# Kernel tuning notes

Measured on AMD Instinct MI355X. Metric: run time of the kernel, lower is better.

The kernel has to match this reference:

```python
import jax, jax.numpy as jnp
import numpy as np

B, S, HID = 2, 2048, 2048
NH, NOPE, ROPE = 16, 128, 64
HD = NOPE + ROPE          # 192
VHD = 128
KVR, QR = 512, 1536
FFN = 5632
THETA = 10000.0
EPS = 1e-6


def rmsnorm(x, w, eps=EPS):
    xf = x.astype(jnp.float32)
    rms = jnp.sqrt(jnp.mean(xf * xf, axis=-1, keepdims=True) + eps)
    return (xf / rms).astype(x.dtype) * w


def apply_rope(x, cos, sin):
    # x: (..., rope_dim); half-split rotation convention
    half = x.shape[-1] // 2
    x1, x2 = x[..., :half], x[..., half:]
    return jnp.concatenate([x1 * cos - x2 * sin, x2 * cos + x1 * sin], axis=-1)


def rope_tables(seq_len, dim, theta=THETA):
    inv_freq = 1.0 / (theta ** (jnp.arange(0, dim, 2, dtype=jnp.float32) / dim))
    t = jnp.arange(seq_len, dtype=jnp.float32)
    freqs = jnp.outer(t, inv_freq)           # (S, dim/2)
    return jnp.cos(freqs), jnp.sin(freqs)


def setup_inputs():
    key = jax.random.key(0)
    ks = jax.random.split(key, 10)
    def w(k, shape, fan_in):
        return jax.random.normal(k, shape, dtype=jnp.float32) * (fan_in ** -0.5)
    return {
        'x': jax.random.normal(ks[0], (B, S, HID), dtype=jnp.float32),
        'attn_norm_w': jnp.ones((HID,), jnp.float32),
        'wq_down': w(ks[1], (HID, QR), HID),
        'wq_up': w(ks[2], (QR, NH * HD), QR),
        'wkv_down': w(ks[3], (HID, KVR + ROPE), HID),
        'kv_norm_w': jnp.ones((KVR,), jnp.float32),
        'wkv_up': w(ks[4], (KVR, NH * (NOPE + VHD)), KVR),
        'wout': w(ks[5], (NH * VHD, HID), NH * VHD),
        'ffn_norm_w': jnp.ones((HID,), jnp.float32),
        'w_gate': w(ks[6], (HID, FFN), HID),
        'w_up': w(ks[7], (HID, FFN), HID),
        'w_down': w(ks[8], (FFN, HID), FFN),
    }


def reference(x, attn_norm_w, wq_down, wq_up, wkv_down, kv_norm_w, wkv_up, wout,
              ffn_norm_w, w_gate, w_up, w_down):
    scale = 1.0 / np.sqrt(HD)
    # --- attention sub-block ---
    h = rmsnorm(x, attn_norm_w)
    q = (h @ wq_down) @ wq_up                       # (B,S,NH*HD)
    q = q.reshape(B, S, NH, HD)
    q_nope, q_rope = q[..., :NOPE], q[..., NOPE:]
    kv_full = h @ wkv_down                          # (B,S,KVR+ROPE)
    kv_c, k_rope = kv_full[..., :KVR], kv_full[..., KVR:]
    kv_c = rmsnorm(kv_c, kv_norm_w)
    kv_exp = (kv_c @ wkv_up).reshape(B, S, NH, NOPE + VHD)
    k_nope, v = kv_exp[..., :NOPE], kv_exp[..., NOPE:]

    cos, sin = rope_tables(S, ROPE)                 # (S, ROPE/2)
    cos4, sin4 = cos[None, :, None, :], sin[None, :, None, :]
    q_rope = apply_rope(q_rope, cos4, sin4)         # (B,S,NH,ROPE)
    k_rope = apply_rope(k_rope[:, :, None, :], cos4, sin4)  # (B,S,1,ROPE)
    k_rope = jnp.broadcast_to(k_rope, (B, S, NH, ROPE))

    q_full = jnp.concatenate([q_nope, q_rope], axis=-1)     # (B,S,NH,HD)
    k = jnp.concatenate([k_nope, k_rope], axis=-1)          # (B,S,NH,HD)

    scores = jnp.einsum('bqhd,bkhd->bhqk', q_full, k) * scale
    causal = jnp.tril(jnp.ones((S, S), dtype=bool))
    scores = jnp.where(causal[None, None], scores, jnp.finfo(scores.dtype).min)
    probs = jax.nn.softmax(scores, axis=-1)
    attn = jnp.einsum('bhqk,bkhd->bqhd', probs, v).reshape(B, S, NH * VHD)
    x = x + attn @ wout

    # --- SwiGLU MLP sub-block ---
    h2 = rmsnorm(x, ffn_norm_w)
    ffn = (jax.nn.silu(h2 @ w_gate) * (h2 @ w_up)) @ w_down
    return x + ffn
```

## Files before the change

kernel.cpp:

```cpp
#include <hip/hip_runtime.h>
#include <hip/hip_bf16.h>


using bf16x8 = __attribute__((ext_vector_type(8))) short;
using f32x4  = __attribute__((ext_vector_type(4))) float;

#define GLOBAL_AS __attribute__((address_space(1)))
#define LDS_AS    __attribute__((address_space(3)))
#define MFMA16(a, b, c) __builtin_amdgcn_mfma_f32_16x16x32_bf16((a), (b), (c), 0, 0, 0)

static constexpr int Sc = 2048;

__device__ __forceinline__ void gload16(const void* g, void* l) {
  __builtin_amdgcn_global_load_lds((const GLOBAL_AS unsigned int*)g,
                                   (LDS_AS unsigned int*)l, 16, 0, 0);
}
__device__ __forceinline__ float bf2f(unsigned short u) {
  union { float f; unsigned int i; } x; x.i = ((unsigned int)u) << 16; return x.f;
}
__device__ __forceinline__ unsigned short f2bf(float f) {
  union { float f; unsigned int i; } x; x.f = f;
  unsigned int i = x.i;
  return (unsigned short)((i + 0x7fffu + ((i >> 16) & 1u)) >> 16);
}
__device__ __forceinline__ int swz4(int r) { return ((r >> 2) & 3) ^ (r & 3); }

__global__ void fill_k(float* out, float v, int n) {
  int i = blockIdx.x * 256 + threadIdx.x;
  if (i < n) out[i] = v;
}

__global__ __launch_bounds__(256) void wtrans(const float* __restrict__ W,
                                              unsigned short* __restrict__ WT,
                                              int K, int N) {
  __shared__ float t[64][65];
  const int n0 = blockIdx.x * 64, k0 = blockIdx.y * 64;
  const int tx = threadIdx.x & 15, ty = threadIdx.x >> 4;
#pragma unroll
  for (int i = 0; i < 4; ++i) {
    int k = k0 + ty + i * 16;
    const float4 v = *(const float4*)(W + (size_t)k * N + n0 + tx * 4);
    t[ty + i * 16][tx * 4 + 0] = v.x;
    t[ty + i * 16][tx * 4 + 1] = v.y;
    t[ty + i * 16][tx * 4 + 2] = v.z;
    t[ty + i * 16][tx * 4 + 3] = v.w;
  }
  __syncthreads();
  const int kx = threadIdx.x & 7, ny = threadIdx.x >> 3;
#pragma unroll
  for (int i = 0; i < 2; ++i) {
    int nl = ny + i * 32;
    unsigned short u[8];
#pragma unroll
    for (int j = 0; j < 8; ++j) u[j] = f2bf(t[kx * 8 + j][nl]);
    *(uint4*)(WT + (size_t)(n0 + nl) * K + k0 + kx * 8) = *(uint4*)u;
  }
}

__global__ void rope_tab(float* __restrict__ cosT, float* __restrict__ sinT) {
  int i = blockIdx.x * 256 + threadIdx.x;
  if (i >= Sc * 32) return;
  int s = i >> 5, j = i & 31;
  float inv = powf(10000.0f, -(float)j / 32.0f);
  float a = (float)s * inv;
  cosT[i] = cosf(a);
  sinT[i] = sinf(a);
}

__global__ __launch_bounds__(256) void rmsnorm_k(const float* __restrict__ in,
                                                 const float* __restrict__ w,
                                                 unsigned short* __restrict__ out,
                                                 int D, int istride, int ostride) {
  const int row = blockIdx.x;
  const float* x = in + (size_t)row * istride;
  float ss = 0.f;
  for (int c = threadIdx.x * 4; c < D; c += 1024) {
    const float4 v = *(const float4*)(x + c);
    ss += v.x * v.x + v.y * v.y + v.z * v.z + v.w * v.w;
  }
#pragma unroll
  for (int off = 1; off < 64; off <<= 1) ss += __shfl_xor(ss, off);
  __shared__ float part[4];
  if ((threadIdx.x & 63) == 0) part[threadIdx.x >> 6] = ss;
  __syncthreads();
  float tot = part[0] + part[1] + part[2] + part[3];
  float r = rsqrtf(tot / (float)D + 1e-6f);
  for (int c = threadIdx.x * 4; c < D; c += 1024) {
    const float4 v = *(const float4*)(x + c);
    ushort4 o;
    o.x = f2bf(v.x * r * w[c + 0]);
    o.y = f2bf(v.y * r * w[c + 1]);
    o.z = f2bf(v.z * r * w[c + 2]);
    o.w = f2bf(v.w * r * w[c + 3]);
    *(ushort4*)(out + (size_t)row * ostride + c) = o;
  }
}

enum { EPI_BF16 = 0, EPI_F32 = 1, EPI_ADDF32 = 2, EPI_SILU = 3 };

template <int EPI>
__global__ __launch_bounds__(256) void gemm_sb1(const unsigned short* __restrict__ A,
                                                const unsigned short* __restrict__ BT,
                                                void* __restrict__ Cp,
                                                const float* __restrict__ resid,
                                                const unsigned short* __restrict__ other,
                                                int M, int N, int K) {
  __shared__ unsigned short ldsA[128 * 64];
  __shared__ unsigned short ldsB[128 * 64];
  const int tid = threadIdx.x;
  const int w = tid >> 6, lane = tid & 63;
  const int rl = lane & 15, gh = lane >> 4;
  const int wm = (w >> 1) * 64, wn = (w & 1) * 64;

  const int nwg = gridDim.x;
  const int orig = blockIdx.x;
  const int qq = nwg >> 3, rr = nwg & 7;
  const int xcd = orig & 7, lidx = orig >> 3;
  const int fswz = (xcd < rr ? xcd * (qq + 1) : rr * (qq + 1) + (xcd - rr) * qq) + lidx;
  const int MT = M >> 7;
  const int m0 = (fswz % MT) * 128;
  const int n0 = (fswz / MT) * 128;

  const unsigned short* sA[4];
  const unsigned short* sB[4];
#pragma unroll
  for (int i = 0; i < 4; ++i) {
    int G = i * 256 + tid, r = G >> 3, sl = (G & 7) ^ (r & 7);
    sA[i] = A + (size_t)(m0 + r) * K + sl * 8;
    sB[i] = BT + (size_t)(n0 + r) * K + sl * 8;
  }
  auto STAGE = [&](int kt) {
    const int ko = kt * 64;
#pragma unroll
    for (int i = 0; i < 4; ++i) {
      gload16(sA[i] + ko, &ldsA[(i * 256 + w * 64) * 8]);
      gload16(sB[i] + ko, &ldsB[(i * 256 + w * 64) * 8]);
    }
  };

  int aoff[4], boff[4];
#pragma unroll
  for (int i = 0; i < 4; ++i) {
    aoff[i] = (wm + i * 16 + rl) * 64;
    boff[i] = (wn + i * 16 + rl) * 64;
  }

  f32x4 acc[4][4] = {};
  const int nk = K >> 6;

  STAGE(0);
  asm volatile("s_waitcnt vmcnt(0)" ::: "memory");
  __builtin_amdgcn_s_barrier();

  for (int kt = 0; kt < nk; ++kt) {
    bf16x8 a[4][2], b[4][2];
#pragma unroll
    for (int i = 0; i < 4; ++i)
#pragma unroll
      for (int ks = 0; ks < 2; ++ks) {
        const int ra = wm + i * 16 + rl;
        a[i][ks] = *(const bf16x8*)&ldsA[aoff[i] + ((((ks << 2) + gh)) ^ (ra & 7)) * 8];
        const int rb = wn + i * 16 + rl;
        b[i][ks] = *(const bf16x8*)&ldsB[boff[i] + ((((ks << 2) + gh)) ^ (rb & 7)) * 8];
      }
    asm volatile("s_waitcnt lgkmcnt(0)" ::: "memory");
    __builtin_amdgcn_sched_barrier(0);
    __builtin_amdgcn_s_setprio(1);
#pragma unroll
    for (int i = 0; i < 4; ++i)
#pragma unroll
      for (int j = 0; j < 4; ++j) acc[i][j] = MFMA16(a[i][0], b[j][0], acc[i][j]);
    __builtin_amdgcn_s_setprio(0);
    __builtin_amdgcn_sched_barrier(0);
    __builtin_amdgcn_s_barrier();
    STAGE((kt + 1 < nk) ? kt + 1 : nk - 1);
    __builtin_amdgcn_sched_barrier(0);
    __builtin_amdgcn_s_setprio(1);
#pragma unroll
    for (int i = 0; i < 4; ++i)
#pragma unroll
      for (int j = 0; j < 4; ++j) acc[i][j] = MFMA16(a[i][1], b[j][1], acc[i][j]);
    __builtin_amdgcn_s_setprio(0);
    __builtin_amdgcn_sched_barrier(0);
    asm volatile("s_waitcnt vmcnt(0)" ::: "memory");
    __builtin_amdgcn_s_barrier();
  }

#pragma unroll
  for (int i = 0; i < 4; ++i) {
#pragma unroll
    for (int j = 0; j < 4; ++j) {
#pragma unroll
      for (int rg = 0; rg < 4; ++rg) {
        const int row = m0 + wm + i * 16 + gh * 4 + rg;
        const int col = n0 + wn + j * 16 + rl;
        const size_t idx = (size_t)row * N + col;
        const float v = acc[i][j][rg];
        if constexpr (EPI == EPI_BF16) {
          ((unsigned short*)Cp)[idx] = f2bf(v);
        } else if constexpr (EPI == EPI_F32) {
          ((float*)Cp)[idx] = v;
        } else if constexpr (EPI == EPI_ADDF32) {
          ((float*)Cp)[idx] = v + resid[idx];
        } else {
          float gv = bf2f(other[idx]);
          float sg = gv / (1.f + __expf(-gv));
          ((unsigned short*)Cp)[idx] = f2bf(sg * v);
        }
      }
    }
  }
}

template <int EPI>
__global__ __launch_bounds__(512) void gemm_sb2(const unsigned short* __restrict__ A,
                                                const unsigned short* __restrict__ BT,
                                                void* __restrict__ Cp,
                                                const float* __restrict__ resid,
                                                const unsigned short* __restrict__ other,
                                                int M, int N, int K) {
  __shared__ unsigned short ldsA[128 * 64];
  __shared__ unsigned short ldsB[256 * 64];
  const int tid = threadIdx.x;
  const int w = tid >> 6, lane = tid & 63;
  const int rl = lane & 15, gh = lane >> 4;
  const int wm = (w >> 2) * 64, wn = (w & 3) * 64;

  const int nwg = gridDim.x;
  const int orig = blockIdx.x;
  const int qq = nwg >> 3, rr = nwg & 7;
  const int xcd = orig & 7, lidx = orig >> 3;
  const int fswz = (xcd < rr ? xcd * (qq + 1) : rr * (qq + 1) + (xcd - rr) * qq) + lidx;
  const int MT = M >> 7;
  const int m0 = (fswz % MT) * 128;
  const int n0 = (fswz / MT) * 256;

  const unsigned short* sA[2];
#pragma unroll
  for (int i = 0; i < 2; ++i) {
    int G = i * 512 + tid, r = G >> 3, sl = (G & 7) ^ (r & 7);
    sA[i] = A + (size_t)(m0 + r) * K + sl * 8;
  }
  const unsigned short* sB[4];
#pragma unroll
  for (int i = 0; i < 4; ++i) {
    int G = i * 512 + tid, r = G >> 3, sl = (G & 7) ^ (r & 7);
    sB[i] = BT + (size_t)(n0 + r) * K + sl * 8;
  }
  auto STAGE = [&](int kt) {
    const int ko = kt * 64;
#pragma unroll
    for (int i = 0; i < 2; ++i)
      gload16(sA[i] + ko, &ldsA[(i * 512 + w * 64) * 8]);
#pragma unroll
    for (int i = 0; i < 4; ++i)
      gload16(sB[i] + ko, &ldsB[(i * 512 + w * 64) * 8]);
  };

  int aoff[4], boff[4];
#pragma unroll
  for (int i = 0; i < 4; ++i) {
    aoff[i] = (wm + i * 16 + rl) * 64;
    boff[i] = (wn + i * 16 + rl) * 64;
  }

  f32x4 acc[4][4] = {};
  const int nk = K >> 6;

  STAGE(0);
  asm volatile("s_waitcnt vmcnt(0)" ::: "memory");
  __builtin_amdgcn_s_barrier();

  for (int kt = 0; kt < nk; ++kt) {
    bf16x8 a[4][2], b[4][2];
#pragma unroll
    for (int i = 0; i < 4; ++i)
#pragma unroll
      for (int ks = 0; ks < 2; ++ks) {
        const int ra = wm + i * 16 + rl;
        a[i][ks] = *(const bf16x8*)&ldsA[aoff[i] + ((((ks << 2) + gh)) ^ (ra & 7)) * 8];
        const int rb = wn + i * 16 + rl;
        b[i][ks] = *(const bf16x8*)&ldsB[boff[i] + ((((ks << 2) + gh)) ^ (rb & 7)) * 8];
      }
    asm volatile("s_waitcnt lgkmcnt(0)" ::: "memory");
    __builtin_amdgcn_sched_barrier(0);
    __builtin_amdgcn_s_setprio(1);
#pragma unroll
    for (int i = 0; i < 4; ++i)
#pragma unroll
      for (int j = 0; j < 4; ++j) acc[i][j] = MFMA16(a[i][0], b[j][0], acc[i][j]);
    __builtin_amdgcn_s_setprio(0);
    __builtin_amdgcn_sched_barrier(0);
    __builtin_amdgcn_s_barrier();
    STAGE((kt + 1 < nk) ? kt + 1 : nk - 1);
    __builtin_amdgcn_sched_barrier(0);
    __builtin_amdgcn_s_setprio(1);
#pragma unroll
    for (int i = 0; i < 4; ++i)
#pragma unroll
      for (int j = 0; j < 4; ++j) acc[i][j] = MFMA16(a[i][1], b[j][1], acc[i][j]);
    __builtin_amdgcn_s_setprio(0);
    __builtin_amdgcn_sched_barrier(0);
    asm volatile("s_waitcnt vmcnt(0)" ::: "memory");
    __builtin_amdgcn_s_barrier();
  }

#pragma unroll
  for (int i = 0; i < 4; ++i) {
#pragma unroll
    for (int j = 0; j < 4; ++j) {
#pragma unroll
      for (int rg = 0; rg < 4; ++rg) {
        const int row = m0 + wm + i * 16 + gh * 4 + rg;
        const int col = n0 + wn + j * 16 + rl;
        const size_t idx = (size_t)row * N + col;
        const float v = acc[i][j][rg];
        if constexpr (EPI == EPI_BF16) {
          ((unsigned short*)Cp)[idx] = f2bf(v);
        } else if constexpr (EPI == EPI_F32) {
          ((float*)Cp)[idx] = v;
        } else if constexpr (EPI == EPI_ADDF32) {
          ((float*)Cp)[idx] = v + resid[idx];
        } else {
          float gv = bf2f(other[idx]);
          float sg = gv / (1.f + __expf(-gv));
          ((unsigned short*)Cp)[idx] = f2bf(sg * v);
        }
      }
    }
  }
}

__global__ __launch_bounds__(256) void repack_q(const unsigned short* __restrict__ q,
                                                const float* __restrict__ cosT,
                                                const float* __restrict__ sinT,
                                                unsigned short* __restrict__ Qc) {
  const int row = blockIdx.x;
  const int b = row >> 11, s = row & 2047;
  const float scale = 0.07216878364870322f;
  const unsigned short* qr = q + (size_t)row * 3072;
  for (int i = threadIdx.x; i < 3072; i += 256) {
    int h = i / 192, d = i - h * 192;
    float v;
    if (d < 128) {
      v = bf2f(qr[h * 192 + d]);
    } else {
      int j = d - 128;
      int jj = j & 31;
      float x1 = bf2f(qr[h * 192 + 128 + jj]);
      float x2 = bf2f(qr[h * 192 + 160 + jj]);
      float c = cosT[s * 32 + jj], sn = sinT[s * 32 + jj];
      v = (j < 32) ? (x1 * c - x2 * sn) : (x2 * c + x1 * sn);
    }
    Qc[((size_t)(b * 16 + h) * Sc + s) * 192 + d] = f2bf(v * scale);
  }
}

__global__ __launch_bounds__(256) void repack_kv(const unsigned short* __restrict__ kvex,
                                                 const float* __restrict__ kvf,
                                                 const float* __restrict__ cosT,
                                                 const float* __restrict__ sinT,
                                                 unsigned short* __restrict__ Kc,
                                                 unsigned short* __restrict__ VT) {
  __shared__ unsigned short vt_lds[32][136];
  const int bid = blockIdx.x;
  const int st = bid & 63;
  const int h = (bid >> 6) & 15;
  const int b = bid >> 10;
  const int s0 = st * 32;
  const int tid = threadIdx.x;
  const size_t KcBase = (size_t)(b * 16 + h) * Sc;
  for (int i = tid; i < 32 * 32; i += 256) {
    int r = i >> 5, g = i & 31;
    uint4 vdat = *(const uint4*)(kvex + (size_t)(b * Sc + s0 + r) * 4096 + h * 256 + g * 8);
    if (g < 16) {
      *(uint4*)(Kc + (KcBase + s0 + r) * 192 + g * 8) = vdat;
    } else {
      *(uint4*)(&vt_lds[r][(g - 16) * 8]) = vdat;
    }
  }
  for (int i = tid; i < 32 * 64; i += 256) {
    int r = i >> 6, d = i & 63;
    int s = s0 + r;
    int jj = d & 31;
    const float* kvrow = kvf + (size_t)(b * Sc + s) * 640;
    float x1 = kvrow[512 + jj], x2 = kvrow[544 + jj];
    float c = cosT[s * 32 + jj], sn = sinT[s * 32 + jj];
    float v = (d < 32) ? (x1 * c - x2 * sn) : (x2 * c + x1 * sn);
    Kc[(KcBase + s) * 192 + 128 + d] = f2bf(v);
  }
  __syncthreads();
  const int f = tid >> 1, sh = (tid & 1) * 16;
  unsigned int vals[8];
#pragma unroll
  for (int k2 = 0; k2 < 8; ++k2) {
    unsigned int lo = vt_lds[sh + 2 * k2][f];
    unsigned int hi = vt_lds[sh + 2 * k2 + 1][f];
    vals[k2] = lo | (hi << 16);
  }
  unsigned short* dst = VT + ((size_t)(b * 16 + h) * 128 + f) * Sc + s0 + sh;
  ((uint4*)dst)[0] = make_uint4(vals[0], vals[1], vals[2], vals[3]);
  ((uint4*)dst)[1] = make_uint4(vals[4], vals[5], vals[6], vals[7]);
}

__global__ __launch_bounds__(512) void attn_k(const unsigned short* __restrict__ Qc,
                                              const unsigned short* __restrict__ Kc,
                                              const unsigned short* __restrict__ VT,
                                              unsigned short* __restrict__ Ob) {
  __shared__ unsigned short lds_k[2][64 * 192];
  __shared__ unsigned short lds_v[2][128 * 64];
  __shared__ __align__(16) unsigned short p_lds[8][16 * 72];
  const int tid = threadIdx.x, w = tid >> 6, lane = tid & 63;
  const int rl = lane & 15, gh = lane >> 4;
  const int bidx = blockIdx.x;
  const int bh = bidx & 31;
  const int qt = 15 - (bidx >> 5);
  const unsigned short* Qh = Qc + (size_t)bh * Sc * 192;
  const unsigned short* Kh = Kc + (size_t)bh * Sc * 192;
  const unsigned short* Vh = VT + (size_t)bh * 128 * Sc;
  const int qr0 = qt * 128 + w * 16;

  bf16x8 qf[6];
#pragma unroll
  for (int kk = 0; kk < 6; ++kk)
    qf[kk] = *(const bf16x8*)(Qh + (size_t)(qr0 + rl) * 192 + kk * 32 + gh * 8);

  f32x4 o[8] = {};
  float mrun[4] = {-1e30f, -1e30f, -1e30f, -1e30f};
  float srun[4] = {0.f, 0.f, 0.f, 0.f};

  int kr[3], kg[3];
#pragma unroll
  for (int j = 0; j < 3; ++j) {
    int G = j * 512 + tid;
    int r = G / 24, gq = G - r * 24;
    kr[j] = r;
    kg[j] = (gq & ~7) | ((gq & 7) ^ (r & 7));
  }
  int vr[2], vg[2];
#pragma unroll
  for (int j = 0; j < 2; ++j) {
    int G = j * 512 + tid;
    int r = G >> 3;
    vr[j] = r;
    vg[j] = (G & 7) ^ (r & 7);
  }

  auto STAGE = [&](int t, int b) {
    const int k0 = t * 64;
#pragma unroll
    for (int j = 0; j < 3; ++j)
      gload16(Kh + (size_t)(k0 + kr[j]) * 192 + kg[j] * 8,
              &lds_k[b][(j * 512 + w * 64) * 8]);
#pragma unroll
    for (int j = 0; j < 2; ++j)
      gload16(Vh + (size_t)vr[j] * Sc + k0 + vg[j] * 8,
              &lds_v[b][(j * 512 + w * 64) * 8]);
  };

  STAGE(0, 0);
  asm volatile("s_waitcnt vmcnt(0)" ::: "memory");
  __builtin_amdgcn_s_barrier();
  __builtin_amdgcn_sched_barrier(0);

  const int nt = 2 * qt + 2;
  int cur = 0;
  for (int t = 0; t < nt; ++t) {
    if (t + 1 < nt) STAGE(t + 1, cur ^ 1);
    const int k0 = t * 64;
    if (k0 <= qr0 + 15) {
      const unsigned short* lk = lds_k[cur];
      const unsigned short* lv = lds_v[cur];
      f32x4 s[4] = {};
      __builtin_amdgcn_s_setprio(1);
#pragma unroll
      for (int kk = 0; kk < 6; ++kk) {
        const int gq = kk * 4 + gh;
#pragma unroll
        for (int ks = 0; ks < 4; ++ks) {
          const int krow = ks * 16 + rl;
          const int ph = (gq & ~7) | ((gq & 7) ^ (krow & 7));
          bf16x8 kf = *(const bf16x8*)&lk[krow * 192 + ph * 8];
          s[ks] = MFMA16(qf[kk], kf, s[ks]);
        }
      }
      __builtin_amdgcn_s_setprio(0);
      if (k0 + 63 > qr0) {
#pragma unroll
        for (int ks = 0; ks < 4; ++ks)
#pragma unroll
          for (int rg = 0; rg < 4; ++rg) {
            int qrow = qr0 + gh * 4 + rg;
            if (k0 + ks * 16 + rl > qrow) s[ks][rg] = -1e30f;
          }
      }
      float tmax[4];
#pragma unroll
      for (int rg = 0; rg < 4; ++rg) {
        float v = fmaxf(fmaxf(s[0][rg], s[1][rg]), fmaxf(s[2][rg], s[3][rg]));
        v = fmaxf(v, __shfl_xor(v, 1));
        v = fmaxf(v, __shfl_xor(v, 2));
        v = fmaxf(v, __shfl_xor(v, 4));
        v = fmaxf(v, __shfl_xor(v, 8));
        tmax[rg] = v;
      }
      int need = !(tmax[0] <= mrun[0] + 8.f && tmax[1] <= mrun[1] + 8.f &&
                   tmax[2] <= mrun[2] + 8.f && tmax[3] <= mrun[3] + 8.f);
      if (__any(need)) {
        float al[4];
#pragma unroll
        for (int rg = 0; rg < 4; ++rg) {
          float mn = fmaxf(mrun[rg], tmax[rg]);
          al[rg] = __expf(mrun[rg] - mn);
          mrun[rg] = mn;
          srun[rg] *= al[rg];
        }
#pragma unroll
        for (int i = 0; i < 8; ++i)
#pragma unroll
          for (int rg = 0; rg < 4; ++rg) o[i][rg] *= al[rg];
      }
      unsigned short* pw = p_lds[w];
#pragma unroll
      for (int ks = 0; ks < 4; ++ks)
#pragma unroll
        for (int rg = 0; rg < 4; ++rg) {
          float p = __expf(s[ks][rg] - mrun[rg]);
          srun[rg] += p;
          pw[(gh * 4 + rg) * 72 + ks * 16 + rl] = f2bf(p);
        }
      bf16x8 pa0 = *(const bf16x8*)&pw[rl * 72 + 0 * 32 + gh * 8];
      bf16x8 pa1 = *(const bf16x8*)&pw[rl * 72 + 1 * 32 + gh * 8];
      __builtin_amdgcn_s_setprio(1);
#pragma unroll
      for (int vf = 0; vf < 8; ++vf) {
        const int row = vf * 16 + rl;
        bf16x8 v0 = *(const bf16x8*)&lv[row * 64 + ((0 * 4 + gh) ^ (row & 7)) * 8];
        o[vf] = MFMA16(pa0, v0, o[vf]);
        bf16x8 v1 = *(const bf16x8*)&lv[row * 64 + ((1 * 4 + gh) ^ (row & 7)) * 8];
        o[vf] = MFMA16(pa1, v1, o[vf]);
      }
      __builtin_amdgcn_s_setprio(0);
    }
    asm volatile("s_waitcnt vmcnt(0)" ::: "memory");
    __builtin_amdgcn_s_barrier();
    __builtin_amdgcn_sched_barrier(0);
    cur ^= 1;
  }
  float rd[4];
#pragma unroll
  for (int rg = 0; rg < 4; ++rg) {
    float rs = srun[rg];
    rs += __shfl_xor(rs, 1);
    rs += __shfl_xor(rs, 2);
    rs += __shfl_xor(rs, 4);
    rs += __shfl_xor(rs, 8);
    rd[rg] = 1.f / rs;
  }
  const int b = bh >> 4, hh = bh & 15;
#pragma unroll
  for (int vf = 0; vf < 8; ++vf) {
#pragma unroll
    for (int rg = 0; rg < 4; ++rg) {
      int srow = qr0 + gh * 4 + rg;
      int col = hh * 128 + vf * 16 + rl;
      Ob[((size_t)(b * Sc) + srow) * 2048 + col] = f2bf(o[vf][rg] * rd[rg]);
    }
  }
}

extern "C" void kernel_launch(void* const* d_in, const int* in_sizes, int n_in,
                              void* d_out, int out_size, void* d_ws, size_t ws_size,
                              hipStream_t stream) {
  (void)in_sizes; (void)n_in;
  const float* x    = (const float*)d_in[0];
  const float* anw  = (const float*)d_in[1];
  const float* wqd  = (const float*)d_in[2];
  const float* wqu  = (const float*)d_in[3];
  const float* wkvd = (const float*)d_in[4];
  const float* kvnw = (const float*)d_in[5];
  const float* wkvu = (const float*)d_in[6];
  const float* wout = (const float*)d_in[7];
  const float* fnw  = (const float*)d_in[8];
  const float* wg   = (const float*)d_in[9];
  const float* wu   = (const float*)d_in[10];
  const float* wd   = (const float*)d_in[11];
  float* out = (float*)d_out;

  char* ws = (char*)d_ws;
  size_t off = 0;
  auto alloc = [&](size_t bytes) -> char* {
    char* p = ws + off;
    off += (bytes + 255) & ~(size_t)255;
    return p;
  };
  unsigned short* wslot = (unsigned short*)alloc(5632ull * 2048 * 2);
  float* cosT           = (float*)alloc(2048ull * 32 * 4);
  float* sinT           = (float*)alloc(2048ull * 32 * 4);
  unsigned short* hbuf  = (unsigned short*)alloc(4096ull * 2048 * 2);
  char* arena           = alloc(4096ull * 1536 * 2 + 4096ull * 3072 * 2);
  float* kvf            = (float*)alloc(4096ull * 640 * 4);
  unsigned short* kvn   = (unsigned short*)alloc(4096ull * 512 * 2);
  unsigned short* Qc    = (unsigned short*)alloc(32ull * 2048 * 192 * 2);
  unsigned short* Kc    = (unsigned short*)alloc(32ull * 2048 * 192 * 2);
  unsigned short* VTb   = (unsigned short*)alloc(32ull * 128 * 2048 * 2);
  const size_t NEED = off;

  if (ws_size < NEED) {
    fill_k<<<dim3((out_size + 255) / 256), dim3(256), 0, stream>>>(
        out, (float)(ws_size >> 20), out_size);
    return;
  }

  unsigned short* qd    = (unsigned short*)arena;
  unsigned short* q     = (unsigned short*)(arena + 4096ull * 1536 * 2);
  unsigned short* kvex  = (unsigned short*)arena;
  unsigned short* h     = hbuf;
  unsigned short* attnb = hbuf;
  unsigned short* h2    = hbuf;
  unsigned short* gbuf  = Qc;
  float* x2             = out;

  dim3 blk(256), blk512(512);
  rope_tab<<<dim3(256), blk, 0, stream>>>(cosT, sinT);
  rmsnorm_k<<<dim3(4096), blk, 0, stream>>>(x, anw, h, 2048, 2048, 2048);

  wtrans<<<dim3(24, 32), blk, 0, stream>>>(wqd, wslot, 2048, 1536);
  gemm_sb2<EPI_BF16><<<dim3(32 * 6), blk512, 0, stream>>>(h, wslot, qd, nullptr, nullptr, 4096, 1536, 2048);
  wtrans<<<dim3(48, 24), blk, 0, stream>>>(wqu, wslot, 1536, 3072);
  gemm_sb2<EPI_BF16><<<dim3(32 * 12), blk512, 0, stream>>>(qd, wslot, q, nullptr, nullptr, 4096, 3072, 1536);
  repack_q<<<dim3(4096), blk, 0, stream>>>(q, cosT, sinT, Qc);

  wtrans<<<dim3(9, 32), blk, 0, stream>>>(wkvd, wslot, 2048, 576);
  gemm_sb1<EPI_F32><<<dim3(32 * 5), blk, 0, stream>>>(h, wslot, kvf, nullptr, nullptr, 4096, 640, 2048);
  rmsnorm_k<<<dim3(4096), blk, 0, stream>>>(kvf, kvnw, kvn, 512, 640, 512);
  wtrans<<<dim3(64, 8), blk, 0, stream>>>(wkvu, wslot, 512, 4096);
  gemm_sb2<EPI_BF16><<<dim3(32 * 16), blk512, 0, stream>>>(kvn, wslot, kvex, nullptr, nullptr, 4096, 4096, 512);
  repack_kv<<<dim3(2048), blk, 0, stream>>>(kvex, kvf, cosT, sinT, Kc, VTb);

  attn_k<<<dim3(512), blk512, 0, stream>>>(Qc, Kc, VTb, attnb);
  wtrans<<<dim3(32, 32), blk, 0, stream>>>(wout, wslot, 2048, 2048);
  gemm_sb2<EPI_ADDF32><<<dim3(32 * 8), blk512, 0, stream>>>(attnb, wslot, x2, x, nullptr, 4096, 2048, 2048);

  rmsnorm_k<<<dim3(4096), blk, 0, stream>>>(x2, fnw, h2, 2048, 2048, 2048);
  wtrans<<<dim3(88, 32), blk, 0, stream>>>(wg, wslot, 2048, 5632);
  gemm_sb2<EPI_BF16><<<dim3(32 * 22), blk512, 0, stream>>>(h2, wslot, gbuf, nullptr, nullptr, 4096, 5632, 2048);
  wtrans<<<dim3(88, 32), blk, 0, stream>>>(wu, wslot, 2048, 5632);
  gemm_sb2<EPI_SILU><<<dim3(32 * 22), blk512, 0, stream>>>(h2, wslot, gbuf, nullptr, gbuf, 4096, 5632, 2048);
  wtrans<<<dim3(32, 88), blk, 0, stream>>>(wd, wslot, 5632, 2048);
  gemm_sb2<EPI_ADDF32><<<dim3(32 * 8), blk512, 0, stream>>>(gbuf, wslot, out, x2, nullptr, 4096, 2048, 5632);
}
```

Before: 846.5 us.

## Fuse gate and up GEMMs into one dual-accumulator kernel; use 128x128 tiles everywhere

Replaces the 128x256 gemm_sb2 kernel with a new gemm_gu kernel. gemm_gu loads one A tile and both the gate and up weight tiles, keeps two accumulator sets, and applies SiLU(gate)*up in its epilogue. This removes the separate gate GEMM pass, the bf16 write and re-read of the gate output, and the second read of h2. All other GEMMs move to the 256-thread gemm_sb1 with 128-wide N tiles and twice as many blocks. Holding two accumulator sets raises register pressure, and dropping the wider tiles lowers data reuse per block.

```diff
diff --git a/kernel.cpp b/kernel.cpp
--- a/kernel.cpp
+++ b/kernel.cpp
@@ -212,19 +212,18 @@
   }
 }
 
-template <int EPI>
-__global__ __launch_bounds__(512) void gemm_sb2(const unsigned short* __restrict__ A,
-                                                const unsigned short* __restrict__ BT,
-                                                void* __restrict__ Cp,
-                                                const float* __restrict__ resid,
-                                                const unsigned short* __restrict__ other,
-                                                int M, int N, int K) {
+__global__ __launch_bounds__(256) void gemm_gu(const unsigned short* __restrict__ A,
+                                               const unsigned short* __restrict__ BG,
+                                               const unsigned short* __restrict__ BU,
+                                               unsigned short* __restrict__ Cp,
+                                               int M, int N, int K) {
   __shared__ unsigned short ldsA[128 * 64];
-  __shared__ unsigned short ldsB[256 * 64];
+  __shared__ unsigned short ldsG[128 * 64];
+  __shared__ unsigned short ldsU[128 * 64];
   const int tid = threadIdx.x;
   const int w = tid >> 6, lane = tid & 63;
   const int rl = lane & 15, gh = lane >> 4;
-  const int wm = (w >> 2) * 64, wn = (w & 3) * 64;
+  const int wm = (w >> 1) * 64, wn = (w & 1) * 64;
 
   const int nwg = gridDim.x;
   const int orig = blockIdx.x;
@@ -233,28 +232,26 @@
   const int fswz = (xcd < rr ? xcd * (qq + 1) : rr * (qq + 1) + (xcd - rr) * qq) + lidx;
   const int MT = M >> 7;
   const int m0 = (fswz % MT) * 128;
-  const int n0 = (fswz / MT) * 256;
-
-  const unsigned short* sA[2];
-#pragma unroll
-  for (int i = 0; i < 2; ++i) {
-    int G = i * 512 + tid, r = G >> 3, sl = (G & 7) ^ (r & 7);
+  const int n0 = (fswz / MT) * 128;
+
+  const unsigned short* sA[4];
+  const unsigned short* sG[4];
+  const unsigned short* sU[4];
+#pragma unroll
+  for (int i = 0; i < 4; ++i) {
+    int G = i * 256 + tid, r = G >> 3, sl = (G & 7) ^ (r & 7);
     sA[i] = A + (size_t)(m0 + r) * K + sl * 8;
-  }
-  const unsigned short* sB[4];
-#pragma unroll
-  for (int i = 0; i < 4; ++i) {
-    int G = i * 512 + tid, r = G >> 3, sl = (G & 7) ^ (r & 7);
-    sB[i] = BT + (size_t)(n0 + r) * K + sl * 8;
+    sG[i] = BG + (size_t)(n0 + r) * K + sl * 8;
+    sU[i] = BU + (size_t)(n0 + r) * K + sl * 8;
   }
   auto STAGE = [&](int kt) {
     const int ko = kt * 64;
 #pragma unroll
-    for (int i = 0; i < 2; ++i)
-      gload16(sA[i] + ko, &ldsA[(i * 512 + w * 64) * 8]);
-#pragma unroll
-    for (int i = 0; i < 4; ++i)
-      gload16(sB[i] + ko, &ldsB[(i * 512 + w * 64) * 8]);
+    for (int i = 0; i < 4; ++i) {
+      gload16(sA[i] + ko, &ldsA[(i * 256 + w * 64) * 8]);
+      gload16(sG[i] + ko, &ldsG[(i * 256 + w * 64) * 8]);
+      gload16(sU[i] + ko, &ldsU[(i * 256 + w * 64) * 8]);
+    }
   };
 
   int aoff[4], boff[4];
@@ -264,7 +261,8 @@
     boff[i] = (wn + i * 16 + rl) * 64;
   }
 
-  f32x4 acc[4][4] = {};
+  f32x4 accg[4][4] = {};
+  f32x4 accu[4][4] = {};
   const int nk = K >> 6;
 
   STAGE(0);
@@ -272,15 +270,18 @@
   __builtin_amdgcn_s_barrier();
 
   for (int kt = 0; kt < nk; ++kt) {
-    bf16x8 a[4][2], b[4][2];
+    bf16x8 a[4][2], g[4][2], u[4][2];
 #pragma unroll
     for (int i = 0; i < 4; ++i)
 #pragma unroll
       for (int ks = 0; ks < 2; ++ks) {
         const int ra = wm + i * 16 + rl;
-        a[i][ks] = *(const bf16x8*)&ldsA[aoff[i] + ((((ks << 2) + gh)) ^ (ra & 7)) * 8];
+        const int sla = ((((ks << 2) + gh)) ^ (ra & 7)) * 8;
+        a[i][ks] = *(const bf16x8*)&ldsA[aoff[i] + sla];
         const int rb = wn + i * 16 + rl;
-        b[i][ks] = *(const bf16x8*)&ldsB[boff[i] + ((((ks << 2) + gh)) ^ (rb & 7)) * 8];
+        const int slb = ((((ks << 2) + gh)) ^ (rb & 7)) * 8;
+        g[i][ks] = *(const bf16x8*)&ldsG[boff[i] + slb];
+        u[i][ks] = *(const bf16x8*)&ldsU[boff[i] + slb];
       }
     asm volatile("s_waitcnt lgkmcnt(0)" ::: "memory");
     __builtin_amdgcn_sched_barrier(0);
@@ -288,7 +289,10 @@
 #pragma unroll
     for (int i = 0; i < 4; ++i)
 #pragma unroll
-      for (int j = 0; j < 4; ++j) acc[i][j] = MFMA16(a[i][0], b[j][0], acc[i][j]);
+      for (int j = 0; j < 4; ++j) {
+        accg[i][j] = MFMA16(a[i][0], g[j][0], accg[i][j]);
+        accu[i][j] = MFMA16(a[i][0], u[j][0], accu[i][j]);
+      }
     __builtin_amdgcn_s_setprio(0);
     __builtin_amdgcn_sched_barrier(0);
     __builtin_amdgcn_s_barrier();
@@ -298,7 +302,10 @@
 #pragma unroll
     for (int i = 0; i < 4; ++i)
 #pragma unroll
-      for (int j = 0; j < 4; ++j) acc[i][j] = MFMA16(a[i][1], b[j][1], acc[i][j]);
+      for (int j = 0; j < 4; ++j) {
+        accg[i][j] = MFMA16(a[i][1], g[j][1], accg[i][j]);
+        accu[i][j] = MFMA16(a[i][1], u[j][1], accu[i][j]);
+      }
     __builtin_amdgcn_s_setprio(0);
     __builtin_amdgcn_sched_barrier(0);
     asm volatile("s_waitcnt vmcnt(0)" ::: "memory");
@@ -313,19 +320,10 @@
       for (int rg = 0; rg < 4; ++rg) {
         const int row = m0 + wm + i * 16 + gh * 4 + rg;
         const int col = n0 + wn + j * 16 + rl;
-        const size_t idx = (size_t)row * N + col;
-        const float v = acc[i][j][rg];
-        if constexpr (EPI == EPI_BF16) {
-          ((unsigned short*)Cp)[idx] = f2bf(v);
-        } else if constexpr (EPI == EPI_F32) {
-          ((float*)Cp)[idx] = v;
-        } else if constexpr (EPI == EPI_ADDF32) {
-          ((float*)Cp)[idx] = v + resid[idx];
-        } else {
-          float gv = bf2f(other[idx]);
-          float sg = gv / (1.f + __expf(-gv));
-          ((unsigned short*)Cp)[idx] = f2bf(sg * v);
-        }
+        const float gv = accg[i][j][rg];
+        const float uv = accu[i][j][rg];
+        const float sg = gv / (1.f + __expf(-gv));
+        Cp[(size_t)row * N + col] = f2bf(sg * uv);
       }
     }
   }
@@ -615,6 +613,7 @@
   unsigned short* qd    = (unsigned short*)arena;
   unsigned short* q     = (unsigned short*)(arena + 4096ull * 1536 * 2);
   unsigned short* kvex  = (unsigned short*)arena;
+  unsigned short* wslot2 = (unsigned short*)arena;
   unsigned short* h     = hbuf;
   unsigned short* attnb = hbuf;
   unsigned short* h2    = hbuf;
@@ -626,27 +625,26 @@
   rmsnorm_k<<<dim3(4096), blk, 0, stream>>>(x, anw, h, 2048, 2048, 2048);
 
   wtrans<<<dim3(24, 32), blk, 0, stream>>>(wqd, wslot, 2048, 1536);
-  gemm_sb2<EPI_BF16><<<dim3(32 * 6), blk512, 0, stream>>>(h, wslot, qd, nullptr, nullptr, 4096, 1536, 2048);
+  gemm_sb1<EPI_BF16><<<dim3(32 * 12), blk, 0, stream>>>(h, wslot, qd, nullptr, nullptr, 4096, 1536, 2048);
   wtrans<<<dim3(48, 24), blk, 0, stream>>>(wqu, wslot, 1536, 3072);
-  gemm_sb2<EPI_BF16><<<dim3(32 * 12), blk512, 0, stream>>>(qd, wslot, q, nullptr, nullptr, 4096, 3072, 1536);
+  gemm_sb1<EPI_BF16><<<dim3(32 * 24), blk, 0, stream>>>(qd, wslot, q, nullptr, nullptr, 4096, 3072, 1536);
   repack_q<<<dim3(4096), blk, 0, stream>>>(q, cosT, sinT, Qc);
 
   wtrans<<<dim3(9, 32), blk, 0, stream>>>(wkvd, wslot, 2048, 576);
   gemm_sb1<EPI_F32><<<dim3(32 * 5), blk, 0, stream>>>(h, wslot, kvf, nullptr, nullptr, 4096, 640, 2048);
   rmsnorm_k<<<dim3(4096), blk, 0, stream>>>(kvf, kvnw, kvn, 512, 640, 512);
   wtrans<<<dim3(64, 8), blk, 0, stream>>>(wkvu, wslot, 512, 4096);
-  gemm_sb2<EPI_BF16><<<dim3(32 * 16), blk512, 0, stream>>>(kvn, wslot, kvex, nullptr, nullptr, 4096, 4096, 512);
+  gemm_sb1<EPI_BF16><<<dim3(32 * 32), blk, 0, stream>>>(kvn, wslot, kvex, nullptr, nullptr, 4096, 4096, 512);
   repack_kv<<<dim3(2048), blk, 0, stream>>>(kvex, kvf, cosT, sinT, Kc, VTb);
 
   attn_k<<<dim3(512), blk512, 0, stream>>>(Qc, Kc, VTb, attnb);
   wtrans<<<dim3(32, 32), blk, 0, stream>>>(wout, wslot, 2048, 2048);
-  gemm_sb2<EPI_ADDF32><<<dim3(32 * 8), blk512, 0, stream>>>(attnb, wslot, x2, x, nullptr, 4096, 2048, 2048);
+  gemm_sb1<EPI_ADDF32><<<dim3(32 * 16), blk, 0, stream>>>(attnb, wslot, x2, x, nullptr, 4096, 2048, 2048);
 
   rmsnorm_k<<<dim3(4096), blk, 0, stream>>>(x2, fnw, h2, 2048, 2048, 2048);
   wtrans<<<dim3(88, 32), blk, 0, stream>>>(wg, wslot, 2048, 5632);
-  gemm_sb2<EPI_BF16><<<dim3(32 * 22), blk512, 0, stream>>>(h2, wslot, gbuf, nullptr, nullptr, 4096, 5632, 2048);
-  wtrans<<<dim3(88, 32), blk, 0, stream>>>(wu, wslot, 2048, 5632);
-  gemm_sb2<EPI_SILU><<<dim3(32 * 22), blk512, 0, stream>>>(h2, wslot, gbuf, nullptr, gbuf, 4096, 5632, 2048);
+  wtrans<<<dim3(88, 32), blk, 0, stream>>>(wu, wslot2, 2048, 5632);
+  gemm_gu<<<dim3(32 * 44), blk, 0, stream>>>(h2, wslot, wslot2, gbuf, 4096, 5632, 2048);
   wtrans<<<dim3(32, 88), blk, 0, stream>>>(wd, wslot, 5632, 2048);
-  gemm_sb2<EPI_ADDF32><<<dim3(32 * 8), blk512, 0, stream>>>(gbuf, wslot, out, x2, nullptr, 4096, 2048, 5632);
-}
+  gemm_sb1<EPI_ADDF32><<<dim3(32 * 16), blk, 0, stream>>>(gbuf, wslot, out, x2, nullptr, 4096, 2048, 5632);
+}
```

Result: slower. 873.1 us (+3.1%).

## Replace 512-thread GEMM with 4-wave 128x256 variant; route most GEMMs to gemm_sb1

Applied to the files above, without the earlier changes.

Converts the 8-wave gemm_sb2 kernel into gemm_sb3, a 4-wave (256-thread) kernel where each wave computes a 64x128 sub-tile, doubling the accumulators and B fragments per wave. Only the gate GEMM uses the new kernel. The other large GEMMs move to the existing 256-thread gemm_sb1 with twice the grid size, which appears to use smaller tiles. The aim is more reuse per wave and better occupancy trade-offs, at the cost of much higher register pressure in gemm_sb3, lower data reuse in gemm_sb1, and more blocks to schedule.

```diff
diff --git a/kernel.cpp b/kernel.cpp
--- a/kernel.cpp
+++ b/kernel.cpp
@@ -213,7 +213,7 @@
 }
 
 template <int EPI>
-__global__ __launch_bounds__(512) void gemm_sb2(const unsigned short* __restrict__ A,
+__global__ __launch_bounds__(256) void gemm_sb3(const unsigned short* __restrict__ A,
                                                 const unsigned short* __restrict__ BT,
                                                 void* __restrict__ Cp,
                                                 const float* __restrict__ resid,
@@ -224,7 +224,7 @@
   const int tid = threadIdx.x;
   const int w = tid >> 6, lane = tid & 63;
   const int rl = lane & 15, gh = lane >> 4;
-  const int wm = (w >> 2) * 64, wn = (w & 3) * 64;
+  const int wm = (w >> 1) * 64, wn = (w & 1) * 128;
 
   const int nwg = gridDim.x;
   const int orig = blockIdx.x;
@@ -235,36 +235,35 @@
   const int m0 = (fswz % MT) * 128;
   const int n0 = (fswz / MT) * 256;
 
-  const unsigned short* sA[2];
-#pragma unroll
-  for (int i = 0; i < 2; ++i) {
-    int G = i * 512 + tid, r = G >> 3, sl = (G & 7) ^ (r & 7);
+  const unsigned short* sA[4];
+  const unsigned short* sB[8];
+#pragma unroll
+  for (int i = 0; i < 4; ++i) {
+    int G = i * 256 + tid, r = G >> 3, sl = (G & 7) ^ (r & 7);
     sA[i] = A + (size_t)(m0 + r) * K + sl * 8;
   }
-  const unsigned short* sB[4];
-#pragma unroll
-  for (int i = 0; i < 4; ++i) {
-    int G = i * 512 + tid, r = G >> 3, sl = (G & 7) ^ (r & 7);
+#pragma unroll
+  for (int i = 0; i < 8; ++i) {
+    int G = i * 256 + tid, r = G >> 3, sl = (G & 7) ^ (r & 7);
     sB[i] = BT + (size_t)(n0 + r) * K + sl * 8;
   }
   auto STAGE = [&](int kt) {
     const int ko = kt * 64;
 #pragma unroll
-    for (int i = 0; i < 2; ++i)
-      gload16(sA[i] + ko, &ldsA[(i * 512 + w * 64) * 8]);
-#pragma unroll
     for (int i = 0; i < 4; ++i)
-      gload16(sB[i] + ko, &ldsB[(i * 512 + w * 64) * 8]);
+      gload16(sA[i] + ko, &ldsA[(i * 256 + w * 64) * 8]);
+#pragma unroll
+    for (int i = 0; i < 8; ++i)
+      gload16(sB[i] + ko, &ldsB[(i * 256 + w * 64) * 8]);
   };
 
-  int aoff[4], boff[4];
-#pragma unroll
-  for (int i = 0; i < 4; ++i) {
-    aoff[i] = (wm + i * 16 + rl) * 64;
-    boff[i] = (wn + i * 16 + rl) * 64;
-  }
-
-  f32x4 acc[4][4] = {};
+  int aoff[4], boff[8];
+#pragma unroll
+  for (int i = 0; i < 4; ++i) aoff[i] = (wm + i * 16 + rl) * 64;
+#pragma unroll
+  for (int j = 0; j < 8; ++j) boff[j] = (wn + j * 16 + rl) * 64;
+
+  f32x4 acc[4][8] = {};
   const int nk = K >> 6;
 
   STAGE(0);
@@ -272,15 +271,20 @@
   __builtin_amdgcn_s_barrier();
 
   for (int kt = 0; kt < nk; ++kt) {
-    bf16x8 a[4][2], b[4][2];
+    bf16x8 a[4][2], b[8][2];
 #pragma unroll
     for (int i = 0; i < 4; ++i)
 #pragma unroll
       for (int ks = 0; ks < 2; ++ks) {
         const int ra = wm + i * 16 + rl;
         a[i][ks] = *(const bf16x8*)&ldsA[aoff[i] + ((((ks << 2) + gh)) ^ (ra & 7)) * 8];
-        const int rb = wn + i * 16 + rl;
-        b[i][ks] = *(const bf16x8*)&ldsB[boff[i] + ((((ks << 2) + gh)) ^ (rb & 7)) * 8];
+      }
+#pragma unroll
+    for (int j = 0; j < 8; ++j)
+#pragma unroll
+      for (int ks = 0; ks < 2; ++ks) {
+        const int rb = wn + j * 16 + rl;
+        b[j][ks] = *(const bf16x8*)&ldsB[boff[j] + ((((ks << 2) + gh)) ^ (rb & 7)) * 8];
       }
     asm volatile("s_waitcnt lgkmcnt(0)" ::: "memory");
     __builtin_amdgcn_sched_barrier(0);
@@ -288,7 +292,7 @@
 #pragma unroll
     for (int i = 0; i < 4; ++i)
 #pragma unroll
-      for (int j = 0; j < 4; ++j) acc[i][j] = MFMA16(a[i][0], b[j][0], acc[i][j]);
+      for (int j = 0; j < 8; ++j) acc[i][j] = MFMA16(a[i][0], b[j][0], acc[i][j]);
     __builtin_amdgcn_s_setprio(0);
     __builtin_amdgcn_sched_barrier(0);
     __builtin_amdgcn_s_barrier();
@@ -298,7 +302,7 @@
 #pragma unroll
     for (int i = 0; i < 4; ++i)
 #pragma unroll
-      for (int j = 0; j < 4; ++j) acc[i][j] = MFMA16(a[i][1], b[j][1], acc[i][j]);
+      for (int j = 0; j < 8; ++j) acc[i][j] = MFMA16(a[i][1], b[j][1], acc[i][j]);
     __builtin_amdgcn_s_setprio(0);
     __builtin_amdgcn_sched_barrier(0);
     asm volatile("s_waitcnt vmcnt(0)" ::: "memory");
@@ -308,7 +312,7 @@
 #pragma unroll
   for (int i = 0; i < 4; ++i) {
 #pragma unroll
-    for (int j = 0; j < 4; ++j) {
+    for (int j = 0; j < 8; ++j) {
 #pragma unroll
       for (int rg = 0; rg < 4; ++rg) {
         const int row = m0 + wm + i * 16 + gh * 4 + rg;
@@ -626,27 +630,27 @@
   rmsnorm_k<<<dim3(4096), blk, 0, stream>>>(x, anw, h, 2048, 2048, 2048);
 
   wtrans<<<dim3(24, 32), blk, 0, stream>>>(wqd, wslot, 2048, 1536);
-  gemm_sb2<EPI_BF16><<<dim3(32 * 6), blk512, 0, stream>>>(h, wslot, qd, nullptr, nullptr, 4096, 1536, 2048);
+  gemm_sb1<EPI_BF16><<<dim3(32 * 12), blk, 0, stream>>>(h, wslot, qd, nullptr, nullptr, 4096, 1536, 2048);
   wtrans<<<dim3(48, 24), blk, 0, stream>>>(wqu, wslot, 1536, 3072);
-  gemm_sb2<EPI_BF16><<<dim3(32 * 12), blk512, 0, stream>>>(qd, wslot, q, nullptr, nullptr, 4096, 3072, 1536);
+  gemm_sb1<EPI_BF16><<<dim3(32 * 24), blk, 0, stream>>>(qd, wslot, q, nullptr, nullptr, 4096, 3072, 1536);
   repack_q<<<dim3(4096), blk, 0, stream>>>(q, cosT, sinT, Qc);
 
   wtrans<<<dim3(9, 32), blk, 0, stream>>>(wkvd, wslot, 2048, 576);
   gemm_sb1<EPI_F32><<<dim3(32 * 5), blk, 0, stream>>>(h, wslot, kvf, nullptr, nullptr, 4096, 640, 2048);
   rmsnorm_k<<<dim3(4096), blk, 0, stream>>>(kvf, kvnw, kvn, 512, 640, 512);
   wtrans<<<dim3(64, 8), blk, 0, stream>>>(wkvu, wslot, 512, 4096);
-  gemm_sb2<EPI_BF16><<<dim3(32 * 16), blk512, 0, stream>>>(kvn, wslot, kvex, nullptr, nullptr, 4096, 4096, 512);
+  gemm_sb1<EPI_BF16><<<dim3(32 * 32), blk, 0, stream>>>(kvn, wslot, kvex, nullptr, nullptr, 4096, 4096, 512);
   repack_kv<<<dim3(2048), blk, 0, stream>>>(kvex, kvf, cosT, sinT, Kc, VTb);
 
   attn_k<<<dim3(512), blk512, 0, stream>>>(Qc, Kc, VTb, attnb);
   wtrans<<<dim3(32, 32), blk, 0, stream>>>(wout, wslot, 2048, 2048);
-  gemm_sb2<EPI_ADDF32><<<dim3(32 * 8), blk512, 0, stream>>>(attnb, wslot, x2, x, nullptr, 4096, 2048, 2048);
+  gemm_sb1<EPI_ADDF32><<<dim3(32 * 16), blk, 0, stream>>>(attnb, wslot, x2, x, nullptr, 4096, 2048, 2048);
 
   rmsnorm_k<<<dim3(4096), blk, 0, stream>>>(x2, fnw, h2, 2048, 2048, 2048);
   wtrans<<<dim3(88, 32), blk, 0, stream>>>(wg, wslot, 2048, 5632);
-  gemm_sb2<EPI_BF16><<<dim3(32 * 22), blk512, 0, stream>>>(h2, wslot, gbuf, nullptr, nullptr, 4096, 5632, 2048);
+  gemm_sb3<EPI_BF16><<<dim3(32 * 22), blk, 0, stream>>>(h2, wslot, gbuf, nullptr, nullptr, 4096, 5632, 2048);
   wtrans<<<dim3(88, 32), blk, 0, stream>>>(wu, wslot, 2048, 5632);
-  gemm_sb2<EPI_SILU><<<dim3(32 * 22), blk512, 0, stream>>>(h2, wslot, gbuf, nullptr, gbuf, 4096, 5632, 2048);
+  gemm_sb1<EPI_SILU><<<dim3(32 * 44), blk, 0, stream>>>(h2, wslot, gbuf, nullptr, gbuf, 4096, 5632, 2048);
   wtrans<<<dim3(32, 88), blk, 0, stream>>>(wd, wslot, 5632, 2048);
-  gemm_sb2<EPI_ADDF32><<<dim3(32 * 8), blk512, 0, stream>>>(gbuf, wslot, out, x2, nullptr, 4096, 2048, 5632);
-}
+  gemm_sb1<EPI_ADDF32><<<dim3(32 * 16), blk, 0, stream>>>(gbuf, wslot, out, x2, nullptr, 4096, 2048, 5632);
+}
```

Result: no change. 833.0 us (-1.6%).

## Replace 128x256 GEMMs with 128x128 tiles and single-buffer attention K tile

Applied to the files above, without the earlier changes.

Swaps the 512-thread 128x256-tile GEMM for the existing 256-thread 128x128 gemm_sb1 on most projections, doubling grid sizes. A new gemm_sb1h variant double-buffers the B tile, and it is used only for the gate GEMM. In the attention kernel the K tile drops from double to single buffering with an extra barrier, which frees LDS and is meant to raise occupancy. Smaller tiles give more workgroups and better CU balance, at the cost of more global traffic per FLOP and an extra synchronization point per attention step.

```diff
diff --git a/kernel.cpp b/kernel.cpp
--- a/kernel.cpp
+++ b/kernel.cpp
@@ -213,18 +213,18 @@
 }
 
 template <int EPI>
-__global__ __launch_bounds__(512) void gemm_sb2(const unsigned short* __restrict__ A,
-                                                const unsigned short* __restrict__ BT,
-                                                void* __restrict__ Cp,
-                                                const float* __restrict__ resid,
-                                                const unsigned short* __restrict__ other,
-                                                int M, int N, int K) {
+__global__ __launch_bounds__(256) void gemm_sb1h(const unsigned short* __restrict__ A,
+                                                 const unsigned short* __restrict__ BT,
+                                                 void* __restrict__ Cp,
+                                                 const float* __restrict__ resid,
+                                                 const unsigned short* __restrict__ other,
+                                                 int M, int N, int K) {
   __shared__ unsigned short ldsA[128 * 64];
-  __shared__ unsigned short ldsB[256 * 64];
+  __shared__ unsigned short ldsB[2][128 * 64];
   const int tid = threadIdx.x;
   const int w = tid >> 6, lane = tid & 63;
   const int rl = lane & 15, gh = lane >> 4;
-  const int wm = (w >> 2) * 64, wn = (w & 3) * 64;
+  const int wm = (w >> 1) * 64, wn = (w & 1) * 64;
 
   const int nwg = gridDim.x;
   const int orig = blockIdx.x;
@@ -233,28 +233,27 @@
   const int fswz = (xcd < rr ? xcd * (qq + 1) : rr * (qq + 1) + (xcd - rr) * qq) + lidx;
   const int MT = M >> 7;
   const int m0 = (fswz % MT) * 128;
-  const int n0 = (fswz / MT) * 256;
-
-  const unsigned short* sA[2];
-#pragma unroll
-  for (int i = 0; i < 2; ++i) {
-    int G = i * 512 + tid, r = G >> 3, sl = (G & 7) ^ (r & 7);
+  const int n0 = (fswz / MT) * 128;
+
+  const unsigned short* sA[4];
+  const unsigned short* sB[4];
+#pragma unroll
+  for (int i = 0; i < 4; ++i) {
+    int G = i * 256 + tid, r = G >> 3, sl = (G & 7) ^ (r & 7);
     sA[i] = A + (size_t)(m0 + r) * K + sl * 8;
-  }
-  const unsigned short* sB[4];
-#pragma unroll
-  for (int i = 0; i < 4; ++i) {
-    int G = i * 512 + tid, r = G >> 3, sl = (G & 7) ^ (r & 7);
     sB[i] = BT + (size_t)(n0 + r) * K + sl * 8;
   }
-  auto STAGE = [&](int kt) {
+  auto STAGE_A = [&](int kt) {
     const int ko = kt * 64;
 #pragma unroll
-    for (int i = 0; i < 2; ++i)
-      gload16(sA[i] + ko, &ldsA[(i * 512 + w * 64) * 8]);
-#pragma unroll
-    for (int i = 0; i < 4; ++i)
-      gload16(sB[i] + ko, &ldsB[(i * 512 + w * 64) * 8]);
+    for (int i = 0; i < 4; ++i)
+      gload16(sA[i] + ko, &ldsA[(i * 256 + w * 64) * 8]);
+  };
+  auto STAGE_B = [&](int kt, int p) {
+    const int ko = kt * 64;
+#pragma unroll
+    for (int i = 0; i < 4; ++i)
+      gload16(sB[i] + ko, &ldsB[p][(i * 256 + w * 64) * 8]);
   };
 
   int aoff[4], boff[4];
@@ -267,11 +266,15 @@
   f32x4 acc[4][4] = {};
   const int nk = K >> 6;
 
-  STAGE(0);
+  STAGE_A(0);
+  STAGE_B(0, 0);
   asm volatile("s_waitcnt vmcnt(0)" ::: "memory");
   __builtin_amdgcn_s_barrier();
 
   for (int kt = 0; kt < nk; ++kt) {
+    const int bcur = kt & 1;
+    STAGE_B((kt + 1 < nk) ? kt + 1 : nk - 1, bcur ^ 1);
+    const unsigned short* lB = &ldsB[bcur][0];
     bf16x8 a[4][2], b[4][2];
 #pragma unroll
     for (int i = 0; i < 4; ++i)
@@ -280,7 +283,7 @@
         const int ra = wm + i * 16 + rl;
         a[i][ks] = *(const bf16x8*)&ldsA[aoff[i] + ((((ks << 2) + gh)) ^ (ra & 7)) * 8];
         const int rb = wn + i * 16 + rl;
-        b[i][ks] = *(const bf16x8*)&ldsB[boff[i] + ((((ks << 2) + gh)) ^ (rb & 7)) * 8];
+        b[i][ks] = *(const bf16x8*)&lB[boff[i] + ((((ks << 2) + gh)) ^ (rb & 7)) * 8];
       }
     asm volatile("s_waitcnt lgkmcnt(0)" ::: "memory");
     __builtin_amdgcn_sched_barrier(0);
@@ -292,7 +295,7 @@
     __builtin_amdgcn_s_setprio(0);
     __builtin_amdgcn_sched_barrier(0);
     __builtin_amdgcn_s_barrier();
-    STAGE((kt + 1 < nk) ? kt + 1 : nk - 1);
+    STAGE_A((kt + 1 < nk) ? kt + 1 : nk - 1);
     __builtin_amdgcn_sched_barrier(0);
     __builtin_amdgcn_s_setprio(1);
 #pragma unroll
@@ -407,7 +410,7 @@
                                               const unsigned short* __restrict__ Kc,
                                               const unsigned short* __restrict__ VT,
                                               unsigned short* __restrict__ Ob) {
-  __shared__ unsigned short lds_k[2][64 * 192];
+  __shared__ unsigned short lds_k[64 * 192];
   __shared__ unsigned short lds_v[2][128 * 64];
   __shared__ __align__(16) unsigned short p_lds[8][16 * 72];
   const int tid = threadIdx.x, w = tid >> 6, lane = tid & 63;
@@ -446,32 +449,35 @@
     vg[j] = (G & 7) ^ (r & 7);
   }
 
-  auto STAGE = [&](int t, int b) {
+  auto STAGE_K = [&](int t) {
     const int k0 = t * 64;
 #pragma unroll
     for (int j = 0; j < 3; ++j)
       gload16(Kh + (size_t)(k0 + kr[j]) * 192 + kg[j] * 8,
-              &lds_k[b][(j * 512 + w * 64) * 8]);
+              &lds_k[(j * 512 + w * 64) * 8]);
+  };
+  auto STAGE_V = [&](int t, int b) {
+    const int k0 = t * 64;
 #pragma unroll
     for (int j = 0; j < 2; ++j)
       gload16(Vh + (size_t)vr[j] * Sc + k0 + vg[j] * 8,
               &lds_v[b][(j * 512 + w * 64) * 8]);
   };
 
-  STAGE(0, 0);
+  STAGE_K(0);
+  STAGE_V(0, 0);
   asm volatile("s_waitcnt vmcnt(0)" ::: "memory");
   __builtin_amdgcn_s_barrier();
   __builtin_amdgcn_sched_barrier(0);
 
   const int nt = 2 * qt + 2;
-  int cur = 0;
+  int vcur = 0;
   for (int t = 0; t < nt; ++t) {
-    if (t + 1 < nt) STAGE(t + 1, cur ^ 1);
+    if (t + 1 < nt) STAGE_V(t + 1, vcur ^ 1);
     const int k0 = t * 64;
-    if (k0 <= qr0 + 15) {
-      const unsigned short* lk = lds_k[cur];
-      const unsigned short* lv = lds_v[cur];
-      f32x4 s[4] = {};
+    const bool docomp = (k0 <= qr0 + 15);
+    f32x4 s[4] = {};
+    if (docomp) {
       __builtin_amdgcn_s_setprio(1);
 #pragma unroll
       for (int kk = 0; kk < 6; ++kk) {
@@ -480,11 +486,18 @@
         for (int ks = 0; ks < 4; ++ks) {
           const int krow = ks * 16 + rl;
           const int ph = (gq & ~7) | ((gq & 7) ^ (krow & 7));
-          bf16x8 kf = *(const bf16x8*)&lk[krow * 192 + ph * 8];
+          bf16x8 kf = *(const bf16x8*)&lds_k[krow * 192 + ph * 8];
           s[ks] = MFMA16(qf[kk], kf, s[ks]);
         }
       }
       __builtin_amdgcn_s_setprio(0);
+      asm volatile("s_waitcnt lgkmcnt(0)" ::: "memory");
+    }
+    __builtin_amdgcn_sched_barrier(0);
+    __builtin_amdgcn_s_barrier();
+    if (t + 1 < nt) STAGE_K(t + 1);
+    __builtin_amdgcn_sched_barrier(0);
+    if (docomp) {
       if (k0 + 63 > qr0) {
 #pragma unroll
         for (int ks = 0; ks < 4; ++ks)
@@ -531,6 +544,7 @@
         }
       bf16x8 pa0 = *(const bf16x8*)&pw[rl * 72 + 0 * 32 + gh * 8];
       bf16x8 pa1 = *(const bf16x8*)&pw[rl * 72 + 1 * 32 + gh * 8];
+      const unsigned short* lv = lds_v[vcur];
       __builtin_amdgcn_s_setprio(1);
 #pragma unroll
       for (int vf = 0; vf < 8; ++vf) {
@@ -545,7 +559,7 @@
     asm volatile("s_waitcnt vmcnt(0)" ::: "memory");
     __builtin_amdgcn_s_barrier();
     __builtin_amdgcn_sched_barrier(0);
-    cur ^= 1;
+    vcur ^= 1;
   }
   float rd[4];
 #pragma unroll
@@ -626,27 +640,27 @@
   rmsnorm_k<<<dim3(4096), blk, 0, stream>>>(x, anw, h, 2048, 2048, 2048);
 
   wtrans<<<dim3(24, 32), blk, 0, stream>>>(wqd, wslot, 2048, 1536);
-  gemm_sb2<EPI_BF16><<<dim3(32 * 6), blk512, 0, stream>>>(h, wslot, qd, nullptr, nullptr, 4096, 1536, 2048);
+  gemm_sb1<EPI_BF16><<<dim3(32 * 12), blk, 0, stream>>>(h, wslot, qd, nullptr, nullptr, 4096, 1536, 2048);
   wtrans<<<dim3(48, 24), blk, 0, stream>>>(wqu, wslot, 1536, 3072);
-  gemm_sb2<EPI_BF16><<<dim3(32 * 12), blk512, 0, stream>>>(qd, wslot, q, nullptr, nullptr, 4096, 3072, 1536);
+  gemm_sb1<EPI_BF16><<<dim3(32 * 24), blk, 0, stream>>>(qd, wslot, q, nullptr, nullptr, 4096, 3072, 1536);
   repack_q<<<dim3(4096), blk, 0, stream>>>(q, cosT, sinT, Qc);
 
   wtrans<<<dim3(9, 32), blk, 0, stream>>>(wkvd, wslot, 2048, 576);
   gemm_sb1<EPI_F32><<<dim3(32 * 5), blk, 0, stream>>>(h, wslot, kvf, nullptr, nullptr, 4096, 640, 2048);
   rmsnorm_k<<<dim3(4096), blk, 0, stream>>>(kvf, kvnw, kvn, 512, 640, 512);
   wtrans<<<dim3(64, 8), blk, 0, stream>>>(wkvu, wslot, 512, 4096);
-  gemm_sb2<EPI_BF16><<<dim3(32 * 16), blk512, 0, stream>>>(kvn, wslot, kvex, nullptr, nullptr, 4096, 4096, 512);
+  gemm_sb1<EPI_BF16><<<dim3(32 * 32), blk, 0, stream>>>(kvn, wslot, kvex, nullptr, nullptr, 4096, 4096, 512);
   repack_kv<<<dim3(2048), blk, 0, stream>>>(kvex, kvf, cosT, sinT, Kc, VTb);
 
   attn_k<<<dim3(512), blk512, 0, stream>>>(Qc, Kc, VTb, attnb);
   wtrans<<<dim3(32, 32), blk, 0, stream>>>(wout, wslot, 2048, 2048);
-  gemm_sb2<EPI_ADDF32><<<dim3(32 * 8), blk512, 0, stream>>>(attnb, wslot, x2, x, nullptr, 4096, 2048, 2048);
+  gemm_sb1<EPI_ADDF32><<<dim3(32 * 16), blk, 0, stream>>>(attnb, wslot, x2, x, nullptr, 4096, 2048, 2048);
 
   rmsnorm_k<<<dim3(4096), blk, 0, stream>>>(x2, fnw, h2, 2048, 2048, 2048);
   wtrans<<<dim3(88, 32), blk, 0, stream>>>(wg, wslot, 2048, 5632);
-  gemm_sb2<EPI_BF16><<<dim3(32 * 22), blk512, 0, stream>>>(h2, wslot, gbuf, nullptr, nullptr, 4096, 5632, 2048);
+  gemm_sb1h<EPI_BF16><<<dim3(32 * 44), blk, 0, stream>>>(h2, wslot, gbuf, nullptr, nullptr, 4096, 5632, 2048);
   wtrans<<<dim3(88, 32), blk, 0, stream>>>(wu, wslot, 2048, 5632);
-  gemm_sb2<EPI_SILU><<<dim3(32 * 22), blk512, 0, stream>>>(h2, wslot, gbuf, nullptr, gbuf, 4096, 5632, 2048);
+  gemm_sb1<EPI_SILU><<<dim3(32 * 44), blk, 0, stream>>>(h2, wslot, gbuf, nullptr, gbuf, 4096, 5632, 2048);
   wtrans<<<dim3(32, 88), blk, 0, stream>>>(wd, wslot, 5632, 2048);
-  gemm_sb2<EPI_ADDF32><<<dim3(32 * 8), blk512, 0, stream>>>(gbuf, wslot, out, x2, nullptr, 4096, 2048, 5632);
-}
+  gemm_sb1<EPI_ADDF32><<<dim3(32 * 16), blk, 0, stream>>>(gbuf, wslot, out, x2, nullptr, 4096, 2048, 5632);
+}
```

New measurement: 755.0 us. -10.8%, faster.
